# Optimization experiments

Hardware: AMD Instinct MI355X
Metric: run time of the kernel (lower is better)

## Reference

```python
import jax, jax.numpy as jnp
import numpy as np
import math

B, S, H, NH = 2, 2048, 1024, 16
DK = H // NH
EPS = 1e-5

def setup_inputs() -> dict:
    key = jax.random.key(0)
    ks = jax.random.split(key, 8)
    sd = 0.02
    return {
        "x": jax.random.normal(ks[0], (B, S, H), dtype=jnp.float32),
        "ln1_w": jnp.ones((H,), jnp.float32),
        "ln1_b": jnp.zeros((H,), jnp.float32),
        "W_qkv": jax.random.normal(ks[1], (H, 3 * H), jnp.float32) * sd,
        "b_qkv": jnp.zeros((3 * H,), jnp.float32),
        "W_o": jax.random.normal(ks[2], (H, H), jnp.float32) * sd,
        "b_o": jnp.zeros((H,), jnp.float32),
        "ln2_w": jnp.ones((H,), jnp.float32),
        "ln2_b": jnp.zeros((H,), jnp.float32),
        "W_fc": jax.random.normal(ks[3], (H, 4 * H), jnp.float32) * sd,
        "b_fc": jnp.zeros((4 * H,), jnp.float32),
        "W_proj": jax.random.normal(ks[4], (4 * H, H), jnp.float32) * sd,
        "b_proj": jnp.zeros((H,), jnp.float32),
    }

def _layernorm(x, w, b):
    mu = jnp.mean(x, axis=-1, keepdims=True)
    var = jnp.mean(jnp.square(x - mu), axis=-1, keepdims=True)
    return (x - mu) * jax.lax.rsqrt(var + EPS) * w + b

def _attn(x, W_qkv, b_qkv, W_o, b_o):
    bs, seq, _ = x.shape
    qkv = x @ W_qkv + b_qkv                      # [b,s,3H]
    q, k, v = jnp.split(qkv, 3, axis=-1)
    q = q.reshape(bs, seq, NH, DK).transpose(0, 2, 1, 3)  # [b,h,s,d]
    k = k.reshape(bs, seq, NH, DK).transpose(0, 2, 1, 3)
    v = v.reshape(bs, seq, NH, DK).transpose(0, 2, 1, 3)
    scores = jnp.einsum("bhqd,bhkd->bhqk", q, k) / math.sqrt(DK)
    causal = jnp.tril(jnp.ones((seq, seq), bool))
    scores = jnp.where(causal, scores, -jnp.inf)
    attn = jax.nn.softmax(scores, axis=-1)
    out = jnp.einsum("bhqk,bhkd->bhqd", attn, v)
    out = out.transpose(0, 2, 1, 3).reshape(bs, seq, H)
    return out @ W_o + b_o

def reference(x, ln1_w, ln1_b, W_qkv, b_qkv, W_o, b_o, ln2_w, ln2_b, W_fc, b_fc, W_proj, b_proj):
    x = x + _attn(_layernorm(x, ln1_w, ln1_b), W_qkv, b_qkv, W_o, b_o)
    h = _layernorm(x, ln2_w, ln2_b)
    h = jax.nn.gelu(h @ W_fc + b_fc, approximate=False) @ W_proj + b_proj
    return x + h
```

## Files before the change

kernel.cpp:

```cpp
#include <hip/hip_runtime.h>
#include <hip/hip_bf16.h>
#include <math.h>

#define H_DIM 1024
#define SEQ   2048
#define BATCH 2
#define NHEAD 16
#define DKV   64
#define ROWS  (BATCH*SEQ)
#define QSCALE 0.18033688f

typedef __attribute__((ext_vector_type(8))) short short8;
typedef __attribute__((ext_vector_type(4))) float f32x4;

static __device__ __forceinline__ unsigned short f32_bf16(float f) {
    unsigned int u = __builtin_bit_cast(unsigned int, f);
    u += 0x7FFF + ((u >> 16) & 1);
    return (unsigned short)(u >> 16);
}

static __device__ __forceinline__ float fast_erf(float x) {
    float ax = fabsf(x);
    float t = 1.0f / fmaf(0.3275911f, ax, 1.0f);
    float p = t * fmaf(t, fmaf(t, fmaf(t, fmaf(t, 1.061405429f, -1.453152027f),
                                       1.421413741f), -0.284496736f), 0.254829592f);
    float y = fmaf(-p, __expf(-ax * ax), 1.0f);
    return copysignf(y, x);
}

static __device__ __forceinline__ void gload16(const unsigned short* g, unsigned short* l) {
    __builtin_amdgcn_global_load_lds(
        (const __attribute__((address_space(1))) void*)g,
        (__attribute__((address_space(3))) void*)l,
        16, 0, 0);
}

__global__ __launch_bounds__(256) void transpose_bf16(const float* __restrict__ in,
                                                      unsigned short* __restrict__ out,
                                                      int K, int N) {
    __shared__ float tile[32][33];
    int n0 = blockIdx.x * 32, k0 = blockIdx.y * 32;
    int tx = threadIdx.x & 31, ty = threadIdx.x >> 5;
    #pragma unroll
    for (int i = 0; i < 4; ++i)
        tile[ty + i * 8][tx] = in[(size_t)(k0 + ty + i * 8) * N + n0 + tx];
    __syncthreads();
    #pragma unroll
    for (int i = 0; i < 4; ++i)
        out[(size_t)(n0 + ty + i * 8) * K + k0 + tx] = f32_bf16(tile[tx][ty + i * 8]);
}

__global__ __launch_bounds__(256) void ln_bf16(const float* __restrict__ x,
                                               const float* __restrict__ w,
                                               const float* __restrict__ bb,
                                               unsigned short* __restrict__ out) {
    int row = blockIdx.x;
    int tid = threadIdx.x;
    float4 v = ((const float4*)(x + (size_t)row * H_DIM))[tid];
    float s  = v.x + v.y + v.z + v.w;
    float s2 = v.x*v.x + v.y*v.y + v.z*v.z + v.w*v.w;
    #pragma unroll
    for (int off = 1; off < 64; off <<= 1) {
        s  += __shfl_xor(s,  off, 64);
        s2 += __shfl_xor(s2, off, 64);
    }
    __shared__ float red[8];
    int wv = tid >> 6;
    if ((tid & 63) == 0) { red[wv] = s; red[4 + wv] = s2; }
    __syncthreads();
    s  = red[0] + red[1] + red[2] + red[3];
    s2 = red[4] + red[5] + red[6] + red[7];
    float mu = s * (1.0f / H_DIM);
    float rs = rsqrtf(s2 * (1.0f / H_DIM) - mu * mu + 1e-5f);
    float4 wv4 = ((const float4*)w)[tid];
    float4 bv4 = ((const float4*)bb)[tid];
    ushort4 o;
    o.x = f32_bf16((v.x - mu) * rs * wv4.x + bv4.x);
    o.y = f32_bf16((v.y - mu) * rs * wv4.y + bv4.y);
    o.z = f32_bf16((v.z - mu) * rs * wv4.z + bv4.z);
    o.w = f32_bf16((v.w - mu) * rs * wv4.w + bv4.w);
    ((ushort4*)(out + (size_t)row * H_DIM))[tid] = o;
}

template<int EPI>
static __device__ __forceinline__ void epi_store(f32x4 a, int row0, int col, int N,
                                                 const float* __restrict__ bias,
                                                 const float* __restrict__ resid,
                                                 float* __restrict__ outF,
                                                 unsigned short* __restrict__ outH,
                                                 unsigned short* __restrict__ outH2) {
    float bv = bias[col];
    if (EPI == 4 && col >= 2048) {
        int bb = row0 >> 11, ss = row0 & 2047;
        int hd = col - 2048;
        ushort4 u;
        u.x = f32_bf16(a[0] + bv);
        u.y = f32_bf16(a[1] + bv);
        u.z = f32_bf16(a[2] + bv);
        u.w = f32_bf16(a[3] + bv);
        *(ushort4*)&outH2[((size_t)bb * 1024 + hd) * SEQ + ss] = u;
    } else {
        #pragma unroll
        for (int j = 0; j < 4; ++j) {
            int row = row0 + j;
            size_t idx = (size_t)row * N + col;
            float c = a[j] + bv;
            if (EPI == 0) {
                outF[idx] = c;
            } else if (EPI == 1) {
                outF[idx] = resid[idx] + c;
            } else if (EPI == 2) {
                float g = 0.5f * c * (1.0f + fast_erf(c * 0.70710678118f));
                outH[idx] = f32_bf16(g);
            } else if (EPI == 3) {
                outH[idx] = f32_bf16(c);
            } else {
                float c2 = (col < 1024) ? c * QSCALE : c;
                outH[(size_t)row * 2048 + col] = f32_bf16(c2);
            }
        }
    }
}

template<int EPI, int NI>
__global__ __launch_bounds__(512) void gemmT(const unsigned short* __restrict__ A,
                                             const unsigned short* __restrict__ Bt,
                                             const float* __restrict__ bias,
                                             const float* __restrict__ resid,
                                             float* __restrict__ outF,
                                             unsigned short* __restrict__ outH,
                                             unsigned short* __restrict__ outH2,
                                             int gx, int N, int K) {
    constexpr int BN = NI * 32;
    constexpr int WN = BN / 4;
    constexpr int NT = WN / 16;
    __shared__ __attribute__((aligned(16))) unsigned short As[128][64];
    __shared__ __attribute__((aligned(16))) unsigned short Bs[BN][64];
    int tid = threadIdx.x;
    int w = tid >> 6, l = tid & 63;
    int l15 = l & 15, lg = l >> 4;
    int wm = w & 1, wn = w >> 1;

    int qq = gridDim.x >> 3;
    int wg = (blockIdx.x & 7) * qq + (blockIdx.x >> 3);
    int bm = wg / gx, bn = wg - bm * gx;
    int m0 = bm * 128, n0 = bn * BN;

    f32x4 acc[4][NT] = {};

    const unsigned short* aptr[2];
    unsigned short* lA[2];
    #pragma unroll
    for (int j = 0; j < 2; ++j) {
        int slot = j * 512 + tid;
        int row = slot >> 3;
        int lchunk = (slot & 7) ^ (row & 7);
        aptr[j] = A + (size_t)(m0 + row) * K + lchunk * 8;
        lA[j] = &As[0][0] + (size_t)slot * 8 - l * 8;
    }
    const unsigned short* bptr[NI / 2];
    unsigned short* lB[NI / 2];
    #pragma unroll
    for (int j = 0; j < NI / 2; ++j) {
        int slot = j * 512 + tid;
        int row = slot >> 3;
        int lchunk = (slot & 7) ^ (row & 7);
        bptr[j] = Bt + (size_t)(n0 + row) * K + lchunk * 8;
        lB[j] = &Bs[0][0] + (size_t)slot * 8 - l * 8;
    }
    int swz[2];
    swz[0] = ((0 + lg) ^ (l15 & 7)) * 8;
    swz[1] = ((4 + lg) ^ (l15 & 7)) * 8;
    const unsigned short* pA = &As[wm * 64 + l15][0];
    const unsigned short* pB = &Bs[wn * WN + l15][0];

    for (int k0 = 0; k0 < K; k0 += 64) {
        __syncthreads();
        #pragma unroll
        for (int j = 0; j < 2; ++j) gload16(aptr[j] + k0, lA[j]);
        #pragma unroll
        for (int j = 0; j < NI / 2; ++j) gload16(bptr[j] + k0, lB[j]);
        __syncthreads();

        #pragma unroll
        for (int ks = 0; ks < 2; ++ks) {
            short8 af[4], bf[NT];
            #pragma unroll
            for (int mi = 0; mi < 4; ++mi)
                af[mi] = *(const short8*)(pA + mi * 16 * 64 + swz[ks]);
            #pragma unroll
            for (int ni = 0; ni < NT; ++ni)
                bf[ni] = *(const short8*)(pB + ni * 16 * 64 + swz[ks]);
            #pragma unroll
            for (int mi = 0; mi < 4; ++mi)
                #pragma unroll
                for (int ni = 0; ni < NT; ++ni)
                    acc[mi][ni] = __builtin_amdgcn_mfma_f32_16x16x32_bf16(af[mi], bf[ni], acc[mi][ni], 0, 0, 0);
        }
    }

    #pragma unroll
    for (int mi = 0; mi < 4; ++mi)
        #pragma unroll
        for (int ni = 0; ni < NT; ++ni)
            epi_store<EPI>(acc[mi][ni], m0 + wm * 64 + mi * 16 + lg * 4,
                           n0 + wn * WN + ni * 16 + l15, N, bias, resid, outF, outH, outH2);
}

__global__ __launch_bounds__(512) void attn_mfma(const unsigned short* __restrict__ qk,
                                                 const unsigned short* __restrict__ vT,
                                                 unsigned short* __restrict__ out) {
    int bid = blockIdx.x;
    int swz = (bid & 7) * 64 + (bid >> 3);
    int b  = swz >> 8;
    int h  = (swz >> 4) & 15;
    int qt = 15 - (swz & 15);
    int tid = threadIdx.x;
    int w = tid >> 6, l = tid & 63;
    int l15 = l & 15, lg = l >> 4;

    __shared__ __attribute__((aligned(16))) unsigned short Ks[64][72];
    __shared__ __attribute__((aligned(16))) unsigned short Vt[64][72];
    __shared__ __attribute__((aligned(16))) unsigned short Ps[8][16][72];

    int qrow = qt * 128 + w * 16 + l15;
    short8 qf[2];
    {
        const unsigned short* qp = qk + (size_t)(b * SEQ + qrow) * 2048 + h * DKV + lg * 8;
        qf[0] = *(const short8*)qp;
        qf[1] = *(const short8*)(qp + 32);
    }
    short8 vf5;
    #pragma unroll
    for (int i = 0; i < 8; ++i) vf5[i] = (l15 == 0) ? (short)0x3F80 : (short)0;

    int srow = tid >> 3;
    int scol = (tid & 7) * 8;
    const unsigned short* kbase = qk + (size_t)(b * SEQ + srow) * 2048 + 1024 + h * DKV + scol;
    const unsigned short* vbase = vT + ((size_t)(b * NHEAD + h) * DKV + srow) * SEQ + scol;

    short8 kr = *(const short8*)kbase;
    short8 vr = *(const short8*)vbase;

    float m = -1e30f;
    f32x4 oacc[4] = {};
    f32x4 oext = {};

    int nt = 2 * qt + 2;
    for (int kt = 0; kt < nt; ++kt) {
        __syncthreads();
        *(short8*)&Ks[srow][scol] = kr;
        *(short8*)&Vt[srow][scol] = vr;
        __syncthreads();
        if (kt + 1 < nt) {
            kr = *(const short8*)(kbase + (size_t)(kt + 1) * 64 * 2048);
            vr = *(const short8*)(vbase + (kt + 1) * 64);
        }

        f32x4 sc[4] = {};
        __builtin_amdgcn_s_setprio(1);
        #pragma unroll
        for (int dstep = 0; dstep < 2; ++dstep) {
            #pragma unroll
            for (int st = 0; st < 4; ++st) {
                short8 kf = *(const short8*)&Ks[st * 16 + l15][dstep * 32 + lg * 8];
                sc[st] = __builtin_amdgcn_mfma_f32_16x16x32_bf16(kf, qf[dstep], sc[st], 0, 0, 0);
            }
        }
        __builtin_amdgcn_s_setprio(0);

        int klim = qrow - kt * 64;
        float pv[4][4];
        float pmax = -1e30f;
        #pragma unroll
        for (int st = 0; st < 4; ++st) {
            #pragma unroll
            for (int j = 0; j < 4; ++j) {
                float s = sc[st][j];
                if (st * 16 + lg * 4 + j > klim) s = -1e30f;
                pv[st][j] = s;
                pmax = fmaxf(pmax, s);
            }
        }

        if (!__all(pmax - m <= 8.0f)) {
            float pr = fmaxf(pmax, __shfl_xor(pmax, 16, 64));
            pr = fmaxf(pr, __shfl_xor(pr, 32, 64));
            float mn = fmaxf(m, pr);
            float scl = exp2f(m - mn);
            #pragma unroll
            for (int d = 0; d < 4; ++d)
                #pragma unroll
                for (int j = 0; j < 4; ++j)
                    oacc[d][j] *= scl;
            #pragma unroll
            for (int j = 0; j < 4; ++j) oext[j] *= scl;
            m = mn;
        }

        #pragma unroll
        for (int st = 0; st < 4; ++st) {
            float p0 = exp2f(pv[st][0] - m);
            float p1 = exp2f(pv[st][1] - m);
            float p2 = exp2f(pv[st][2] - m);
            float p3 = exp2f(pv[st][3] - m);
            unsigned int ua, ub;
            asm("v_cvt_pk_bf16_f32 %0, %1, %2" : "=v"(ua) : "v"(p0), "v"(p1));
            asm("v_cvt_pk_bf16_f32 %0, %1, %2" : "=v"(ub) : "v"(p2), "v"(p3));
            uint2 u = make_uint2(ua, ub);
            *(uint2*)&Ps[w][l15][st * 16 + lg * 4] = u;
        }

        __builtin_amdgcn_s_setprio(1);
        #pragma unroll
        for (int ks = 0; ks < 2; ++ks) {
            short8 pf = *(const short8*)&Ps[w][l15][ks * 32 + lg * 8];
            #pragma unroll
            for (int d = 0; d < 4; ++d) {
                short8 vf = *(const short8*)&Vt[d * 16 + l15][ks * 32 + lg * 8];
                oacc[d] = __builtin_amdgcn_mfma_f32_16x16x32_bf16(vf, pf, oacc[d], 0, 0, 0);
            }
            oext = __builtin_amdgcn_mfma_f32_16x16x32_bf16(vf5, pf, oext, 0, 0, 0);
        }
        __builtin_amdgcn_s_setprio(0);
    }

    float lsum = __shfl(oext[0], l15, 64);
    float inv = 1.0f / lsum;
    size_t ob = (size_t)(b * SEQ + qrow) * H_DIM + h * DKV;
    #pragma unroll
    for (int d = 0; d < 4; ++d) {
        ushort4 u;
        #pragma unroll
        for (int j = 0; j < 4; ++j)
            ((unsigned short*)&u)[j] = f32_bf16(oacc[d][j] * inv);
        *(ushort4*)&out[ob + d * 16 + lg * 4] = u;
    }
}

extern "C" void kernel_launch(void* const* d_in, const int* in_sizes, int n_in,
                              void* d_out, int out_size, void* d_ws, size_t ws_size,
                              hipStream_t stream) {
    const float* x     = (const float*)d_in[0];
    const float* ln1w  = (const float*)d_in[1];
    const float* ln1b  = (const float*)d_in[2];
    const float* Wqkv  = (const float*)d_in[3];
    const float* bqkv  = (const float*)d_in[4];
    const float* Wo    = (const float*)d_in[5];
    const float* bo    = (const float*)d_in[6];
    const float* ln2w  = (const float*)d_in[7];
    const float* ln2b  = (const float*)d_in[8];
    const float* Wfc   = (const float*)d_in[9];
    const float* bfc   = (const float*)d_in[10];
    const float* Wproj = (const float*)d_in[11];
    const float* bproj = (const float*)d_in[12];
    float* out = (float*)d_out;

    char* ws = (char*)d_ws;
    size_t off = 0;
    auto take = [&](size_t bytes) {
        void* p = ws + off;
        off += (bytes + 255) & ~(size_t)255;
        return p;
    };

    unsigned short* WqT  = (unsigned short*)take((size_t)3072 * 1024 * 2);
    unsigned short* WoT  = (unsigned short*)take((size_t)1024 * 1024 * 2);
    unsigned short* WfcT = (unsigned short*)take((size_t)4096 * 1024 * 2);
    unsigned short* WpT  = (unsigned short*)take((size_t)1024 * 4096 * 2);
    unsigned short* xn1   = (unsigned short*)take((size_t)ROWS * 1024 * 2);
    unsigned short* qk_h  = (unsigned short*)take((size_t)ROWS * 2048 * 2);
    unsigned short* vT    = (unsigned short*)take((size_t)ROWS * 1024 * 2);
    unsigned short* attn  = (unsigned short*)take((size_t)ROWS * 1024 * 2);
    float*          x1    = (float*)take((size_t)ROWS * 1024 * 4);
    unsigned short* xn2   = (unsigned short*)take((size_t)ROWS * 1024 * 2);
    unsigned short* hbuf  = (unsigned short*)take((size_t)ROWS * 4096 * 2);

    transpose_bf16<<<dim3(3072 / 32, 1024 / 32), 256, 0, stream>>>(Wqkv,  WqT,  1024, 3072);
    transpose_bf16<<<dim3(1024 / 32, 1024 / 32), 256, 0, stream>>>(Wo,    WoT,  1024, 1024);
    transpose_bf16<<<dim3(4096 / 32, 1024 / 32), 256, 0, stream>>>(Wfc,   WfcT, 1024, 4096);
    transpose_bf16<<<dim3(1024 / 32, 4096 / 32), 256, 0, stream>>>(Wproj, WpT,  4096, 1024);

    ln_bf16<<<ROWS, 256, 0, stream>>>(x, ln1w, ln1b, xn1);

    gemmT<4, 4><<<768, 512, 0, stream>>>(xn1, WqT, bqkv, nullptr, nullptr, qk_h, vT, 24, 3072, 1024);

    attn_mfma<<<512, 512, 0, stream>>>(qk_h, vT, attn);

    gemmT<1, 2><<<512, 512, 0, stream>>>(attn, WoT, bo, x, x1, nullptr, nullptr, 16, 1024, 1024);

    ln_bf16<<<ROWS, 256, 0, stream>>>(x1, ln2w, ln2b, xn2);

    gemmT<2, 4><<<1024, 512, 0, stream>>>(xn2, WfcT, bfc, nullptr, nullptr, hbuf, nullptr, 32, 4096, 1024);

    gemmT<1, 2><<<512, 512, 0, stream>>>(hbuf, WpT, bproj, x1, out, nullptr, nullptr, 16, 1024, 4096);
}
```

Measured before the change: 248.8 us.

## Double-buffer K/V tiles in attention with XOR-swizzled shared memory

```diff
diff --git a/kernel.cpp b/kernel.cpp
--- a/kernel.cpp
+++ b/kernel.cpp
@@ -219,8 +219,8 @@
     int w = tid >> 6, l = tid & 63;
     int l15 = l & 15, lg = l >> 4;
 
-    __shared__ __attribute__((aligned(16))) unsigned short Ks[64][72];
-    __shared__ __attribute__((aligned(16))) unsigned short Vt[64][72];
+    __shared__ __attribute__((aligned(16))) unsigned short Ks[2][64][64];
+    __shared__ __attribute__((aligned(16))) unsigned short Vt[2][64][64];
     __shared__ __attribute__((aligned(16))) unsigned short Ps[8][16][72];
 
     int qrow = qt * 128 + w * 16 + l15;
@@ -235,95 +235,113 @@
     for (int i = 0; i < 8; ++i) vf5[i] = (l15 == 0) ? (short)0x3F80 : (short)0;
 
     int srow = tid >> 3;
-    int scol = (tid & 7) * 8;
-    const unsigned short* kbase = qk + (size_t)(b * SEQ + srow) * 2048 + 1024 + h * DKV + scol;
-    const unsigned short* vbase = vT + ((size_t)(b * NHEAD + h) * DKV + srow) * SEQ + scol;
-
-    short8 kr = *(const short8*)kbase;
-    short8 vr = *(const short8*)vbase;
+    int scl  = (tid & 7) * 8;
+    int spc  = (((tid & 7) ^ (srow & 7)) * 8);
+    const unsigned short* kbase = qk + (size_t)(b * SEQ + srow) * 2048 + 1024 + h * DKV + scl;
+    const unsigned short* vbase = vT + ((size_t)(b * NHEAD + h) * DKV + srow) * SEQ + scl;
+
+    int rk0 = ((0 * 4 + lg) ^ (l15 & 7)) * 8;
+    int rk1 = ((1 * 4 + lg) ^ (l15 & 7)) * 8;
 
     float m = -1e30f;
     f32x4 oacc[4] = {};
     f32x4 oext = {};
 
     int nt = 2 * qt + 2;
-    for (int kt = 0; kt < nt; ++kt) {
+
+    short8 kr0 = *(const short8*)kbase;
+    short8 vr0 = *(const short8*)vbase;
+    *(short8*)&Ks[0][srow][spc] = kr0;
+    *(short8*)&Vt[0][srow][spc] = vr0;
+    short8 kr1 = *(const short8*)(kbase + (size_t)64 * 2048);
+    short8 vr1 = *(const short8*)(vbase + 64);
+    __syncthreads();
+
+#define ATTN_COMPUTE(BUF, KT)                                                          \
+    {                                                                                  \
+        f32x4 sc[4] = {};                                                              \
+        __builtin_amdgcn_s_setprio(1);                                                 \
+        _Pragma("unroll")                                                              \
+        for (int st = 0; st < 4; ++st) {                                               \
+            short8 kf0 = *(const short8*)&Ks[BUF][st * 16 + l15][rk0];                 \
+            sc[st] = __builtin_amdgcn_mfma_f32_16x16x32_bf16(kf0, qf[0], sc[st], 0, 0, 0); \
+            short8 kf1 = *(const short8*)&Ks[BUF][st * 16 + l15][rk1];                 \
+            sc[st] = __builtin_amdgcn_mfma_f32_16x16x32_bf16(kf1, qf[1], sc[st], 0, 0, 0); \
+        }                                                                              \
+        __builtin_amdgcn_s_setprio(0);                                                 \
+        int klim = qrow - (KT) * 64;                                                   \
+        float pv[4][4];                                                                \
+        float pmax = -1e30f;                                                           \
+        _Pragma("unroll")                                                              \
+        for (int st = 0; st < 4; ++st) {                                               \
+            _Pragma("unroll")                                                          \
+            for (int j = 0; j < 4; ++j) {                                              \
+                float s = sc[st][j];                                                   \
+                if (st * 16 + lg * 4 + j > klim) s = -1e30f;                           \
+                pv[st][j] = s;                                                         \
+                pmax = fmaxf(pmax, s);                                                 \
+            }                                                                          \
+        }                                                                              \
+        if (!__all(pmax - m <= 8.0f)) {                                                \
+            float pr = fmaxf(pmax, __shfl_xor(pmax, 16, 64));                          \
+            pr = fmaxf(pr, __shfl_xor(pr, 32, 64));                                    \
+            float mn = fmaxf(m, pr);                                                   \
+            float scl2 = exp2f(m - mn);                                                \
+            _Pragma("unroll")                                                          \
+            for (int d = 0; d < 4; ++d)                                                \
+                _Pragma("unroll")                                                      \
+                for (int j = 0; j < 4; ++j)                                            \
+                    oacc[d][j] *= scl2;                                                \
+            _Pragma("unroll")                                                          \
+            for (int j = 0; j < 4; ++j) oext[j] *= scl2;                               \
+            m = mn;                                                                    \
+        }                                                                              \
+        _Pragma("unroll")                                                              \
+        for (int st = 0; st < 4; ++st) {                                               \
+            float p0 = exp2f(pv[st][0] - m);                                           \
+            float p1 = exp2f(pv[st][1] - m);                                           \
+            float p2 = exp2f(pv[st][2] - m);                                           \
+            float p3 = exp2f(pv[st][3] - m);                                           \
+            unsigned int ua, ub;                                                       \
+            asm("v_cvt_pk_bf16_f32 %0, %1, %2" : "=v"(ua) : "v"(p0), "v"(p1));         \
+            asm("v_cvt_pk_bf16_f32 %0, %1, %2" : "=v"(ub) : "v"(p2), "v"(p3));         \
+            uint2 u = make_uint2(ua, ub);                                              \
+            *(uint2*)&Ps[w][l15][st * 16 + lg * 4] = u;                                \
+        }                                                                              \
+        __builtin_amdgcn_s_setprio(1);                                                 \
+        _Pragma("unroll")                                                              \
+        for (int ks = 0; ks < 2; ++ks) {                                               \
+            short8 pf = *(const short8*)&Ps[w][l15][ks * 32 + lg * 8];                 \
+            int rv = (ks == 0) ? rk0 : rk1;                                            \
+            _Pragma("unroll")                                                          \
+            for (int d = 0; d < 4; ++d) {                                              \
+                short8 vf = *(const short8*)&Vt[BUF][d * 16 + l15][rv];                \
+                oacc[d] = __builtin_amdgcn_mfma_f32_16x16x32_bf16(vf, pf, oacc[d], 0, 0, 0); \
+            }                                                                          \
+            oext = __builtin_amdgcn_mfma_f32_16x16x32_bf16(vf5, pf, oext, 0, 0, 0);    \
+        }                                                                              \
+        __builtin_amdgcn_s_setprio(0);                                                 \
+    }
+
+    for (int t = 0; t < nt; t += 2) {
+        *(short8*)&Ks[1][srow][spc] = kr1;
+        *(short8*)&Vt[1][srow][spc] = vr1;
+        if (t + 2 < nt) {
+            kr0 = *(const short8*)(kbase + (size_t)(t + 2) * 64 * 2048);
+            vr0 = *(const short8*)(vbase + (t + 2) * 64);
+        }
+        ATTN_COMPUTE(0, t);
         __syncthreads();
-        *(short8*)&Ks[srow][scol] = kr;
-        *(short8*)&Vt[srow][scol] = vr;
+        if (t + 2 < nt) {
+            *(short8*)&Ks[0][srow][spc] = kr0;
+            *(short8*)&Vt[0][srow][spc] = vr0;
+            kr1 = *(const short8*)(kbase + (size_t)(t + 3) * 64 * 2048);
+            vr1 = *(const short8*)(vbase + (t + 3) * 64);
+        }
+        ATTN_COMPUTE(1, t + 1);
         __syncthreads();
-        if (kt + 1 < nt) {
-            kr = *(const short8*)(kbase + (size_t)(kt + 1) * 64 * 2048);
-            vr = *(const short8*)(vbase + (kt + 1) * 64);
-        }
-
-        f32x4 sc[4] = {};
-        __builtin_amdgcn_s_setprio(1);
-        #pragma unroll
-        for (int dstep = 0; dstep < 2; ++dstep) {
-            #pragma unroll
-            for (int st = 0; st < 4; ++st) {
-                short8 kf = *(const short8*)&Ks[st * 16 + l15][dstep * 32 + lg * 8];
-                sc[st] = __builtin_amdgcn_mfma_f32_16x16x32_bf16(kf, qf[dstep], sc[st], 0, 0, 0);
-            }
-        }
-        __builtin_amdgcn_s_setprio(0);
-
-        int klim = qrow - kt * 64;
-        float pv[4][4];
-        float pmax = -1e30f;
-        #pragma unroll
-        for (int st = 0; st < 4; ++st) {
-            #pragma unroll
-            for (int j = 0; j < 4; ++j) {
-                float s = sc[st][j];
-                if (st * 16 + lg * 4 + j > klim) s = -1e30f;
-                pv[st][j] = s;
-                pmax = fmaxf(pmax, s);
-            }
-        }
-
-        if (!__all(pmax - m <= 8.0f)) {
-            float pr = fmaxf(pmax, __shfl_xor(pmax, 16, 64));
-            pr = fmaxf(pr, __shfl_xor(pr, 32, 64));
-            float mn = fmaxf(m, pr);
-            float scl = exp2f(m - mn);
-            #pragma unroll
-            for (int d = 0; d < 4; ++d)
-                #pragma unroll
-                for (int j = 0; j < 4; ++j)
-                    oacc[d][j] *= scl;
-            #pragma unroll
-            for (int j = 0; j < 4; ++j) oext[j] *= scl;
-            m = mn;
-        }
-
-        #pragma unroll
-        for (int st = 0; st < 4; ++st) {
-            float p0 = exp2f(pv[st][0] - m);
-            float p1 = exp2f(pv[st][1] - m);
-            float p2 = exp2f(pv[st][2] - m);
-            float p3 = exp2f(pv[st][3] - m);
-            unsigned int ua, ub;
-            asm("v_cvt_pk_bf16_f32 %0, %1, %2" : "=v"(ua) : "v"(p0), "v"(p1));
-            asm("v_cvt_pk_bf16_f32 %0, %1, %2" : "=v"(ub) : "v"(p2), "v"(p3));
-            uint2 u = make_uint2(ua, ub);
-            *(uint2*)&Ps[w][l15][st * 16 + lg * 4] = u;
-        }
-
-        __builtin_amdgcn_s_setprio(1);
-        #pragma unroll
-        for (int ks = 0; ks < 2; ++ks) {
-            short8 pf = *(const short8*)&Ps[w][l15][ks * 32 + lg * 8];
-            #pragma unroll
-            for (int d = 0; d < 4; ++d) {
-                short8 vf = *(const short8*)&Vt[d * 16 + l15][ks * 32 + lg * 8];
-                oacc[d] = __builtin_amdgcn_mfma_f32_16x16x32_bf16(vf, pf, oacc[d], 0, 0, 0);
-            }
-            oext = __builtin_amdgcn_mfma_f32_16x16x32_bf16(vf5, pf, oext, 0, 0, 0);
-        }
-        __builtin_amdgcn_s_setprio(0);
-    }
+    }
+#undef ATTN_COMPUTE
 
     float lsum = __shfl(oext[0], l15, 64);
     float inv = 1.0f / lsum;
```

After: 242.9 us. -2.4%, faster.
